# Performance work log

Hardware: AMD Instinct MI355X
Metric: run time of the kernel (lower is better)

## Reference

```python
import jax, jax.numpy as jnp
import numpy as np
import math

B, S, D, H, NH = 4, 2048, 1024, 1024, 16
HD = H // NH


def setup_inputs() -> dict:
    key = jax.random.key(0)
    ks = jax.random.split(key, 8)
    scale_in = math.sqrt(6.0 / (D + H))   # xavier_uniform for [H, D] linear weights
    scale_out = math.sqrt(6.0 / (H + D))
    return {
        "q": jax.random.normal(ks[0], (B, S, D), jnp.float32),
        "k": jax.random.normal(ks[1], (B, S, D), jnp.float32),
        "v": jax.random.normal(ks[2], (B, S, D), jnp.float32),
        "padding_mask": jnp.zeros((B, S), dtype=bool),
        "W_q": jax.random.uniform(ks[3], (H, D), jnp.float32, -scale_in, scale_in),
        "b_q": jnp.zeros((H,), jnp.float32),
        "W_k": jax.random.uniform(ks[4], (H, D), jnp.float32, -scale_in, scale_in),
        "b_k": jnp.zeros((H,), jnp.float32),
        "W_v": jax.random.uniform(ks[5], (H, D), jnp.float32, -scale_in, scale_in),
        "b_v": jnp.zeros((H,), jnp.float32),
        "W_o": jax.random.uniform(ks[6], (D, H), jnp.float32, -scale_out, scale_out),
        "b_o": jnp.zeros((D,), jnp.float32),
    }


def reference(q, k, v, padding_mask, W_q, b_q, W_k, b_k, W_v, b_v, W_o, b_o):
    b = q.shape[0]
    # projections (torch Linear: x @ W.T + b)
    Q = (q @ W_q.T + b_q).reshape(b, -1, NH, HD).transpose(0, 2, 1, 3)  # [B,NH,S,HD]
    K = (k @ W_k.T + b_k).reshape(b, -1, NH, HD).transpose(0, 2, 1, 3)
    V = (v @ W_v.T + b_v).reshape(b, -1, NH, HD).transpose(0, 2, 1, 3)

    scores = jnp.einsum("bhqd,bhkd->bhqk", Q, K) / math.sqrt(HD)  # [B,NH,S,S]
    sq = scores.shape[-2]
    causal = jnp.triu(jnp.ones((sq, sq), dtype=bool), k=1)
    scores = jnp.where(causal, -jnp.inf, scores)
    scores = jnp.where(padding_mask[:, None, None, :], -jnp.inf, scores)

    attn = jax.nn.softmax(scores, axis=-1)  # dropout p=0.0 -> identity
    out = jnp.einsum("bhqk,bhkd->bhqd", attn, V)
    out = out.transpose(0, 2, 1, 3).reshape(b, -1, H)
    return out @ W_o.T + b_o
```

## Files before the change

kernel.cpp:

```cpp
#include <hip/hip_runtime.h>
#include <hip/hip_bf16.h>
#include <math.h>

typedef __attribute__((ext_vector_type(4))) float f32x4;
typedef __attribute__((ext_vector_type(16))) float f32x16;
typedef __attribute__((ext_vector_type(8))) short short8;
typedef __attribute__((ext_vector_type(4))) unsigned short ushort4_t;
typedef __attribute__((ext_vector_type(4))) unsigned int u32x4;

#define B_  4
#define S_  2048
#define D_  1024
#define NH_ 16
#define HD_ 64

__device__ __forceinline__ unsigned short f2bf(float f) {
  unsigned u = __builtin_bit_cast(unsigned, f);
  u += 0x7FFFu + ((u >> 16) & 1u);
  return (unsigned short)(u >> 16);
}

__device__ __forceinline__ float bf2f(unsigned short s) {
  unsigned u = ((unsigned)s) << 16;
  return __builtin_bit_cast(float, u);
}

__device__ __forceinline__ void gload_lds16(const void* g, void* l) {
  __builtin_amdgcn_global_load_lds(
      (const __attribute__((address_space(1))) unsigned int*)g,
      (__attribute__((address_space(3))) unsigned int*)l, 16, 0, 0);
}

__device__ __forceinline__ unsigned cvt_pk_bf16(float lo, float hi) {
  unsigned r;
  asm("v_cvt_pk_bf16_f32 %0, %1, %2" : "=v"(r) : "v"(lo), "v"(hi));
  return r;
}

__global__ void cvt_bf16_all(
    const float* __restrict__ q, const float* __restrict__ k,
    const float* __restrict__ v, const float* __restrict__ wq,
    const float* __restrict__ wk, const float* __restrict__ wv,
    const float* __restrict__ wo,
    unsigned short* __restrict__ oq, unsigned short* __restrict__ ok,
    unsigned short* __restrict__ ov, unsigned short* __restrict__ owq,
    unsigned short* __restrict__ owk, unsigned short* __restrict__ owv,
    unsigned short* __restrict__ owo) {
  const int y = blockIdx.y;
  const float* in;
  unsigned short* out;
  int n4;
  switch (y) {
    case 0: in = q;  out = oq;  n4 = B_ * S_ * D_ / 4; break;
    case 1: in = k;  out = ok;  n4 = B_ * S_ * D_ / 4; break;
    case 2: in = v;  out = ov;  n4 = B_ * S_ * D_ / 4; break;
    case 3: in = wq; out = owq; n4 = 1024 * 1024 / 4;  break;
    case 4: in = wk; out = owk; n4 = 1024 * 1024 / 4;  break;
    case 5: in = wv; out = owv; n4 = 1024 * 1024 / 4;  break;
    default: in = wo; out = owo; n4 = 1024 * 1024 / 4; break;
  }
  for (int i = blockIdx.x * 256 + threadIdx.x; i < n4; i += 1024 * 256) {
    const float4 f = reinterpret_cast<const float4*>(in)[i];
    ushort4_t r;
    r.x = f2bf(f.x); r.y = f2bf(f.y); r.z = f2bf(f.z); r.w = f2bf(f.w);
    reinterpret_cast<ushort4_t*>(out)[i] = r;
  }
}

template <int OUT_F32>
__device__ __forceinline__ void gemm_body(
    const unsigned short* __restrict__ A,
    const unsigned short* __restrict__ W,
    const float* __restrict__ bias,
    void* __restrict__ Cout, int trans, float oscale,
    unsigned short* At, unsigned short* Wt, int m0, int n0) {
  constexpr int K = 1024;
  const int tid = threadIdx.x;
  const int wave = tid >> 6, lane = tid & 63;
  f32x4 acc[4][4] = {};

  const int srow = tid >> 3;
  const int scol8 = tid & 7;

  for (int kt = 0; kt < K; kt += 64) {
#pragma unroll
    for (int c = 0; c < 4; ++c) {
      const int row = c * 32 + srow;
      const int col = (scol8 ^ (row & 7)) << 3;
      gload_lds16(A + (size_t)(m0 + row) * K + kt + col,
                  (char*)At + c * 4096 + wave * 1024);
    }
#pragma unroll
    for (int c = 0; c < 4; ++c) {
      const int row = c * 32 + srow;
      const int col = (scol8 ^ (row & 7)) << 3;
      gload_lds16(W + (size_t)(n0 + row) * K + kt + col,
                  (char*)Wt + c * 4096 + wave * 1024);
    }
    asm volatile("s_waitcnt vmcnt(0)" ::: "memory");
    __syncthreads();

    const int wr = (wave >> 1) * 64, wc = (wave & 1) * 64;
#pragma unroll
    for (int kk = 0; kk < 2; ++kk) {
      short8 af[4], wf[4];
#pragma unroll
      for (int m = 0; m < 4; ++m) {
        const int row = wr + m * 16 + (lane & 15);
        const int colb = ((kk * 32 + (lane >> 4) * 8) * 2) ^ ((row & 7) << 4);
        af[m] = *(const short8*)((const char*)At + row * 128 + colb);
      }
#pragma unroll
      for (int n = 0; n < 4; ++n) {
        const int row = wc + n * 16 + (lane & 15);
        const int colb = ((kk * 32 + (lane >> 4) * 8) * 2) ^ ((row & 7) << 4);
        wf[n] = *(const short8*)((const char*)Wt + row * 128 + colb);
      }
#pragma unroll
      for (int m = 0; m < 4; ++m)
#pragma unroll
        for (int n = 0; n < 4; ++n)
          acc[m][n] = __builtin_amdgcn_mfma_f32_16x16x32_bf16(af[m], wf[n], acc[m][n], 0, 0, 0);
    }
    __syncthreads();
  }

  const int wr = (wave >> 1) * 64, wc = (wave & 1) * 64;
  const int g = lane >> 4, cl = lane & 15;
#pragma unroll
  for (int m = 0; m < 4; ++m) {
#pragma unroll
    for (int n = 0; n < 4; ++n) {
      const int ng = n0 + wc + n * 16 + cl;
      const float bv = bias[ng];
      if (trans) {
        const int mg = m0 + wr + m * 16 + g * 4;
        const int bb = mg >> 11;
        const int ss = mg & 2047;
        ushort4_t pk;
        pk.x = f2bf(acc[m][n][0] + bv);
        pk.y = f2bf(acc[m][n][1] + bv);
        pk.z = f2bf(acc[m][n][2] + bv);
        pk.w = f2bf(acc[m][n][3] + bv);
        *(ushort4_t*)((unsigned short*)Cout + ((size_t)bb * 1024 + ng) * 2048 + ss) = pk;
      } else {
#pragma unroll
        for (int r = 0; r < 4; ++r) {
          const int mg = m0 + wr + m * 16 + g * 4 + r;
          const float v = (acc[m][n][r] + bv) * oscale;
          if (OUT_F32)
            ((float*)Cout)[(size_t)mg * 1024 + ng] = v;
          else
            ((unsigned short*)Cout)[(size_t)mg * 1024 + ng] = f2bf(v);
        }
      }
    }
  }
}

__global__ __launch_bounds__(256) void gemm_qkv(
    const unsigned short* __restrict__ qb, const unsigned short* __restrict__ kb,
    const unsigned short* __restrict__ vb,
    const unsigned short* __restrict__ Wqb, const unsigned short* __restrict__ Wkb,
    const unsigned short* __restrict__ Wvb,
    const float* __restrict__ bq, const float* __restrict__ bk,
    const float* __restrict__ bv,
    unsigned short* __restrict__ Qp, unsigned short* __restrict__ Kp,
    unsigned short* __restrict__ Vt) {
  __shared__ unsigned short At[128 * 64];
  __shared__ unsigned short Wt[128 * 64];
  const int fl = (int)blockIdx.x + 8 * (int)blockIdx.y + 512 * (int)blockIdx.z;
  const int o  = (fl & 7) * 192 + (fl >> 3);
  const int x = o & 7, y = (o >> 3) & 63, z = o >> 9;
  const unsigned short* A = z == 0 ? qb : (z == 1 ? kb : vb);
  const unsigned short* W = z == 0 ? Wqb : (z == 1 ? Wkb : Wvb);
  const float* bias = z == 0 ? bq : (z == 1 ? bk : bv);
  void* out = z == 0 ? (void*)Qp : (z == 1 ? (void*)Kp : (void*)Vt);
  const float sc = z == 0 ? 0.125f * 1.44269504088896f : 1.0f;
  gemm_body<0>(A, W, bias, out, z == 2, sc, At, Wt, y * 128, x * 128);
}

__global__ __launch_bounds__(256) void gemm_o(
    const unsigned short* __restrict__ A, const unsigned short* __restrict__ W,
    const float* __restrict__ bias, float* __restrict__ out) {
  __shared__ unsigned short At[128 * 64];
  __shared__ unsigned short Wt[128 * 64];
  const int fl = (int)blockIdx.x + 8 * (int)blockIdx.y;
  const int o  = (fl & 7) * 64 + (fl >> 3);
  const int x = o & 7, y = o >> 3;
  gemm_body<1>(A, W, bias, out, 0, 1.0f, At, Wt, y * 128, x * 128);
}

__global__ __launch_bounds__(256) void attn_fwd(
    const unsigned short* __restrict__ Qp,
    const unsigned short* __restrict__ Kp,
    const unsigned short* __restrict__ Vt,
    const unsigned char* __restrict__ pmask,
    unsigned short* __restrict__ Out) {
  __shared__ unsigned short Kt[2][64 * 64];
  __shared__ unsigned short Vl[2][64 * 64];
  __shared__ unsigned char mskA[2048];

  const int tid = threadIdx.x;
  const int wave = tid >> 6, lane = tid & 63;
  const int ql = lane & 31, hi = lane >> 5;
  const int fl = (int)blockIdx.x + 8 * (int)blockIdx.y;
  const int o  = (fl & 7) * 64 + (fl >> 3);
  const int qx = o & 7, bh = o >> 3;
  const int b = bh >> 4, h = bh & 15;
  const int srow = tid >> 3, scol8 = tid & 7;

  *(uint2*)(mskA + tid * 8) = *(const uint2*)(pmask + b * S_ + tid * 8);
  asm volatile("s_waitcnt lgkmcnt(0)" ::: "memory");
  __builtin_amdgcn_s_barrier();

#pragma unroll 1
  for (int half = 0; half < 2; ++half) {
    const int qtile = half ? (15 - qx) : qx;
    const int q0 = qtile * 128;
    const int qw = q0 + wave * 32;
    const int qg = qw + ql;
    const int nt = 2 * qtile + 2;

    auto STAGE = [&](int bi, int t) {
      const int kv0s = t * 64;
#pragma unroll
      for (int c = 0; c < 2; ++c) {
        const int row = c * 32 + srow;
        const int col = (scol8 ^ (row & 7)) << 3;
        gload_lds16(Kp + (size_t)(b * S_ + kv0s + row) * D_ + h * HD_ + col,
                    (char*)Kt[bi] + c * 4096 + wave * 1024);
        gload_lds16(Vt + ((size_t)b * D_ + h * HD_ + row) * S_ + kv0s + col,
                    (char*)Vl[bi] + c * 4096 + wave * 1024);
      }
    };

    short8 qf[4];
#pragma unroll
    for (int s = 0; s < 4; ++s)
      qf[s] = *(const short8*)(Qp + (size_t)(b * S_ + qg) * D_ +
                               h * HD_ + s * 16 + hi * 8);

    float lrow = 0.f;
    f32x16 oacc[2] = {};

    STAGE(0, 0);
    int cur = 0;
#pragma unroll 1
    for (int t = 0; t < nt; ++t) {
      if (t + 1 < nt) {
        STAGE(cur ^ 1, t + 1);
        asm volatile("s_waitcnt vmcnt(4)" ::: "memory");
      } else {
        asm volatile("s_waitcnt vmcnt(0)" ::: "memory");
      }
      __builtin_amdgcn_s_barrier();

      const int kv0 = t * 64;
      const bool active = (kv0 <= qw + 31);
      if (active) {
        const char* KtC = (const char*)Kt[cur];
        const char* VlC = (const char*)Vl[cur];

        f32x16 st[2] = {};
        __builtin_amdgcn_s_setprio(1);
#pragma unroll
        for (int tt = 0; tt < 2; ++tt) {
#pragma unroll
          for (int s = 0; s < 4; ++s) {
            const int row = tt * 32 + ql;
            const int colb = (s * 32 + hi * 16) ^ ((row & 7) << 4);
            const short8 kf = *(const short8*)(KtC + row * 128 + colb);
            st[tt] = __builtin_amdgcn_mfma_f32_32x32x16_bf16(kf, qf[s], st[tt], 0, 0, 0);
          }
        }
        __builtin_amdgcn_s_setprio(0);

        if (__any(mskA[kv0 + lane])) {
#pragma unroll
          for (int tt = 0; tt < 2; ++tt)
#pragma unroll
            for (int r = 0; r < 16; ++r) {
              const int kv = kv0 + tt * 32 + (r & 3) + 8 * (r >> 2) + 4 * hi;
              if (mskA[kv]) st[tt][r] = -1e30f;
            }
        }
        if (kv0 + 63 > qw) {
          const int kvb = kv0 + 4 * hi;
#pragma unroll
          for (int tt = 0; tt < 2; ++tt)
#pragma unroll
            for (int r = 0; r < 16; ++r) {
              const int kv = kvb + tt * 32 + (r & 3) + 8 * (r >> 2);
              st[tt][r] = (kv > qg) ? -1e30f : st[tt][r];
            }
        }

        float rs = 0.f;
#pragma unroll
        for (int tt = 0; tt < 2; ++tt)
#pragma unroll
          for (int r = 0; r < 16; ++r) {
            const float p = exp2f(st[tt][r]);
            st[tt][r] = p;
            rs += p;
          }
        lrow += rs + __shfl_xor(rs, 32, 64);

        short8 pa[4];
#pragma unroll
        for (int tt = 0; tt < 2; ++tt) {
          unsigned c0 = cvt_pk_bf16(st[tt][0],  st[tt][1]);
          unsigned c1 = cvt_pk_bf16(st[tt][2],  st[tt][3]);
          unsigned c2 = cvt_pk_bf16(st[tt][4],  st[tt][5]);
          unsigned c3 = cvt_pk_bf16(st[tt][6],  st[tt][7]);
          unsigned c4 = cvt_pk_bf16(st[tt][8],  st[tt][9]);
          unsigned c5 = cvt_pk_bf16(st[tt][10], st[tt][11]);
          unsigned c6 = cvt_pk_bf16(st[tt][12], st[tt][13]);
          unsigned c7 = cvt_pk_bf16(st[tt][14], st[tt][15]);
          asm("v_permlane32_swap_b32 %0, %1" : "+v"(c0), "+v"(c2));
          asm("v_permlane32_swap_b32 %0, %1" : "+v"(c1), "+v"(c3));
          asm("v_permlane32_swap_b32 %0, %1" : "+v"(c4), "+v"(c6));
          asm("v_permlane32_swap_b32 %0, %1" : "+v"(c5), "+v"(c7));
          u32x4 w0 = {c0, c1, c2, c3};
          u32x4 w1 = {c4, c5, c6, c7};
          pa[2 * tt]     = __builtin_bit_cast(short8, w0);
          pa[2 * tt + 1] = __builtin_bit_cast(short8, w1);
        }

        __builtin_amdgcn_s_setprio(1);
#pragma unroll
        for (int dt = 0; dt < 2; ++dt) {
#pragma unroll
          for (int ks = 0; ks < 4; ++ks) {
            const int row = dt * 32 + ql;
            const int colb = (ks * 32 + hi * 16) ^ ((row & 7) << 4);
            const short8 vf = *(const short8*)(VlC + row * 128 + colb);
            oacc[dt] = __builtin_amdgcn_mfma_f32_32x32x16_bf16(pa[ks], vf, oacc[dt], 0, 0, 0);
          }
        }
        __builtin_amdgcn_s_setprio(0);
      }
      __builtin_amdgcn_s_barrier();
      cur ^= 1;
    }

    const float inv = 1.f / lrow;
#pragma unroll
    for (int r = 0; r < 16; ++r) {
      const int crow = (r & 3) + 8 * (r >> 2) + 4 * hi;
      const float iv = __shfl(inv, crow, 64);
      const size_t base = (size_t)(b * S_ + qw + crow) * 1024 + h * HD_;
      Out[base + ql]      = f2bf(oacc[0][r] * iv);
      Out[base + 32 + ql] = f2bf(oacc[1][r] * iv);
    }
  }
}

extern "C" void kernel_launch(void* const* d_in, const int* in_sizes, int n_in,
                              void* d_out, int out_size, void* d_ws, size_t ws_size,
                              hipStream_t stream) {
  (void)in_sizes; (void)n_in; (void)out_size; (void)ws_size;
  const float* q  = (const float*)d_in[0];
  const float* k  = (const float*)d_in[1];
  const float* v  = (const float*)d_in[2];
  const unsigned char* pm = (const unsigned char*)d_in[3];
  const float* Wq = (const float*)d_in[4];
  const float* bq = (const float*)d_in[5];
  const float* Wk = (const float*)d_in[6];
  const float* bk = (const float*)d_in[7];
  const float* Wv = (const float*)d_in[8];
  const float* bv = (const float*)d_in[9];
  const float* Wo = (const float*)d_in[10];
  const float* bo = (const float*)d_in[11];

  char* ws = (char*)d_ws;
  const size_t MB = 1024 * 1024;
  unsigned short* qb  = (unsigned short*)(ws + 0 * MB);
  unsigned short* kb  = (unsigned short*)(ws + 16 * MB);
  unsigned short* vb  = (unsigned short*)(ws + 32 * MB);
  unsigned short* Wqb = (unsigned short*)(ws + 48 * MB);
  unsigned short* Wkb = (unsigned short*)(ws + 50 * MB);
  unsigned short* Wvb = (unsigned short*)(ws + 52 * MB);
  unsigned short* Wob = (unsigned short*)(ws + 54 * MB);
  unsigned short* Qp  = (unsigned short*)(ws + 56 * MB);
  unsigned short* Kp  = (unsigned short*)(ws + 72 * MB);
  unsigned short* Vt  = (unsigned short*)(ws + 88 * MB);
  unsigned short* AO  = (unsigned short*)(ws + 104 * MB);

  cvt_bf16_all<<<dim3(1024, 7), dim3(256), 0, stream>>>(
      q, k, v, Wq, Wk, Wv, Wo, qb, kb, vb, Wqb, Wkb, Wvb, Wob);

  gemm_qkv<<<dim3(8, 64, 3), dim3(256), 0, stream>>>(qb, kb, vb, Wqb, Wkb, Wvb,
                                                     bq, bk, bv, Qp, Kp, Vt);

  attn_fwd<<<dim3(8, 64), dim3(256), 0, stream>>>(Qp, Kp, Vt, pm, AO);

  gemm_o<<<dim3(8, 64), dim3(256), 0, stream>>>(AO, Wob, bo, (float*)d_out);
}
```

Measured before the change: 195.0 us.

## Stage 128-wide KV tiles in attention and use raw v_exp_f32

The attention kernel now stages K/V tiles of 128 keys per pipeline step, processed as two 64-key sub-chunks, which halves the number of barriers and waits per row tile. Global source addresses are precomputed once per thread. The V layout gets a wider XOR swizzle to match the 256-byte rows. The kernel also checks once whether any padding is present instead of testing each tile, uses the v_exp_f32 instruction directly in place of exp2f, and splits the row-sum across four accumulators. LDS use doubles, which may lower occupancy, and causal tiles at the diagonal may load keys they never use.

```diff
diff --git a/kernel.cpp b/kernel.cpp
--- a/kernel.cpp
+++ b/kernel.cpp
@@ -23,6 +23,12 @@
 __device__ __forceinline__ float bf2f(unsigned short s) {
   unsigned u = ((unsigned)s) << 16;
   return __builtin_bit_cast(float, u);
+}
+
+__device__ __forceinline__ float fexp2(float x) {
+  float r;
+  asm("v_exp_f32 %0, %1" : "=v"(r) : "v"(x));
+  return r;
 }
 
 __device__ __forceinline__ void gload_lds16(const void* g, void* l) {
@@ -197,8 +203,8 @@
     const unsigned short* __restrict__ Vt,
     const unsigned char* __restrict__ pmask,
     unsigned short* __restrict__ Out) {
-  __shared__ unsigned short Kt[2][64 * 64];
-  __shared__ unsigned short Vl[2][64 * 64];
+  __shared__ unsigned short Kt[2][128 * 64];
+  __shared__ unsigned short Vl[2][64 * 128];
   __shared__ unsigned char mskA[2048];
 
   const int tid = threadIdx.x;
@@ -208,11 +214,30 @@
   const int o  = (fl & 7) * 64 + (fl >> 3);
   const int qx = o & 7, bh = o >> 3;
   const int b = bh >> 4, h = bh & 15;
-  const int srow = tid >> 3, scol8 = tid & 7;
 
   *(uint2*)(mskA + tid * 8) = *(const uint2*)(pmask + b * S_ + tid * 8);
   asm volatile("s_waitcnt lgkmcnt(0)" ::: "memory");
   __builtin_amdgcn_s_barrier();
+
+  bool anymask;
+  {
+    const u32x4 m0 = *(const u32x4*)(mskA + lane * 32);
+    const u32x4 m1 = *(const u32x4*)(mskA + lane * 32 + 16);
+    const unsigned orv = m0[0] | m0[1] | m0[2] | m0[3] | m1[0] | m1[1] | m1[2] | m1[3];
+    anymask = __any(orv != 0);
+  }
+
+  const unsigned short* kbase[4];
+  const unsigned short* vbase[4];
+#pragma unroll
+  for (int c = 0; c < 4; ++c) {
+    const int krow = c * 32 + (tid >> 3);
+    const int kcol = ((tid & 7) ^ (krow & 7)) << 3;
+    kbase[c] = Kp + (size_t)(b * S_ + krow) * D_ + h * HD_ + kcol;
+    const int vrow = c * 16 + (tid >> 4);
+    const int vcol = ((tid & 15) ^ (vrow & 15)) << 3;
+    vbase[c] = Vt + ((size_t)b * D_ + h * HD_ + vrow) * S_ + vcol;
+  }
 
 #pragma unroll 1
   for (int half = 0; half < 2; ++half) {
@@ -220,18 +245,15 @@
     const int q0 = qtile * 128;
     const int qw = q0 + wave * 32;
     const int qg = qw + ql;
-    const int nt = 2 * qtile + 2;
+    const int nt = qtile + 1;
 
     auto STAGE = [&](int bi, int t) {
-      const int kv0s = t * 64;
-#pragma unroll
-      for (int c = 0; c < 2; ++c) {
-        const int row = c * 32 + srow;
-        const int col = (scol8 ^ (row & 7)) << 3;
-        gload_lds16(Kp + (size_t)(b * S_ + kv0s + row) * D_ + h * HD_ + col,
-                    (char*)Kt[bi] + c * 4096 + wave * 1024);
-        gload_lds16(Vt + ((size_t)b * D_ + h * HD_ + row) * S_ + kv0s + col,
-                    (char*)Vl[bi] + c * 4096 + wave * 1024);
+      const size_t ko = (size_t)t * 128 * D_;
+      const size_t vo = (size_t)t * 128;
+#pragma unroll
+      for (int c = 0; c < 4; ++c) {
+        gload_lds16(kbase[c] + ko, (char*)Kt[bi] + c * 4096 + wave * 1024);
+        gload_lds16(vbase[c] + vo, (char*)Vl[bi] + c * 4096 + wave * 1024);
       }
     };
 
@@ -250,17 +272,19 @@
     for (int t = 0; t < nt; ++t) {
       if (t + 1 < nt) {
         STAGE(cur ^ 1, t + 1);
-        asm volatile("s_waitcnt vmcnt(4)" ::: "memory");
+        asm volatile("s_waitcnt vmcnt(8)" ::: "memory");
       } else {
         asm volatile("s_waitcnt vmcnt(0)" ::: "memory");
       }
       __builtin_amdgcn_s_barrier();
 
-      const int kv0 = t * 64;
-      const bool active = (kv0 <= qw + 31);
-      if (active) {
-        const char* KtC = (const char*)Kt[cur];
-        const char* VlC = (const char*)Vl[cur];
+      const char* KtC = (const char*)Kt[cur];
+      const char* VlC = (const char*)Vl[cur];
+
+#pragma unroll
+      for (int j = 0; j < 2; ++j) {
+        const int kvc = t * 128 + j * 64;
+        if (kvc > qw + 31) continue;
 
         f32x16 st[2] = {};
         __builtin_amdgcn_s_setprio(1);
@@ -268,7 +292,7 @@
         for (int tt = 0; tt < 2; ++tt) {
 #pragma unroll
           for (int s = 0; s < 4; ++s) {
-            const int row = tt * 32 + ql;
+            const int row = j * 64 + tt * 32 + ql;
             const int colb = (s * 32 + hi * 16) ^ ((row & 7) << 4);
             const short8 kf = *(const short8*)(KtC + row * 128 + colb);
             st[tt] = __builtin_amdgcn_mfma_f32_32x32x16_bf16(kf, qf[s], st[tt], 0, 0, 0);
@@ -276,17 +300,17 @@
         }
         __builtin_amdgcn_s_setprio(0);
 
-        if (__any(mskA[kv0 + lane])) {
+        if (anymask) {
 #pragma unroll
           for (int tt = 0; tt < 2; ++tt)
 #pragma unroll
             for (int r = 0; r < 16; ++r) {
-              const int kv = kv0 + tt * 32 + (r & 3) + 8 * (r >> 2) + 4 * hi;
+              const int kv = kvc + tt * 32 + (r & 3) + 8 * (r >> 2) + 4 * hi;
               if (mskA[kv]) st[tt][r] = -1e30f;
             }
         }
-        if (kv0 + 63 > qw) {
-          const int kvb = kv0 + 4 * hi;
+        if (kvc + 63 > qw) {
+          const int kvb = kvc + 4 * hi;
 #pragma unroll
           for (int tt = 0; tt < 2; ++tt)
 #pragma unroll
@@ -296,15 +320,19 @@
             }
         }
 
-        float rs = 0.f;
+        float rs0 = 0.f, rs1 = 0.f, rs2 = 0.f, rs3 = 0.f;
 #pragma unroll
         for (int tt = 0; tt < 2; ++tt)
 #pragma unroll
           for (int r = 0; r < 16; ++r) {
-            const float p = exp2f(st[tt][r]);
+            const float p = fexp2(st[tt][r]);
             st[tt][r] = p;
-            rs += p;
+            if ((r & 3) == 0) rs0 += p;
+            else if ((r & 3) == 1) rs1 += p;
+            else if ((r & 3) == 2) rs2 += p;
+            else rs3 += p;
           }
+        const float rs = (rs0 + rs1) + (rs2 + rs3);
         lrow += rs + __shfl_xor(rs, 32, 64);
 
         short8 pa[4];
@@ -333,9 +361,9 @@
         for (int dt = 0; dt < 2; ++dt) {
 #pragma unroll
           for (int ks = 0; ks < 4; ++ks) {
-            const int row = dt * 32 + ql;
-            const int colb = (ks * 32 + hi * 16) ^ ((row & 7) << 4);
-            const short8 vf = *(const short8*)(VlC + row * 128 + colb);
+            const int vrow = dt * 32 + ql;
+            const int vcolb = (j * 128 + ks * 32 + hi * 16) ^ ((vrow & 15) << 4);
+            const short8 vf = *(const short8*)(VlC + vrow * 256 + vcolb);
             oacc[dt] = __builtin_amdgcn_mfma_f32_32x32x16_bf16(pa[ks], vf, oacc[dt], 0, 0, 0);
           }
         }
```

Measured after the change: 179.1 us. 8.2% less time.
